# Performance work log

Measured on AMD Instinct MI355X. Metric: run time of the kernel, lower is better.

Reference implementation:

```python
import jax, jax.numpy as jnp
import numpy as np

THR = 1.0  # snntorch Leaky default threshold
BETA = 0.9


def setup_inputs() -> dict:
    key = jax.random.key(0)
    k_in, k_w1, k_b1, k_w2, k_b2 = jax.random.split(key, 5)
    T, B, D, H = 100, 256, 784, 256
    # binary spike train input (rate-coded)
    spike_input = (jax.random.uniform(k_in, (T, B, D)) < 0.5).astype(jnp.float32)
    # nn.Linear init: U(-1/sqrt(fan_in), 1/sqrt(fan_in))
    lim1 = 1.0 / np.sqrt(D)
    lim2 = 1.0 / np.sqrt(H)
    W1 = jax.random.uniform(k_w1, (H, D), minval=-lim1, maxval=lim1, dtype=jnp.float32)
    b1 = jax.random.uniform(k_b1, (H,), minval=-lim1, maxval=lim1, dtype=jnp.float32)
    W2 = jax.random.uniform(k_w2, (D, H), minval=-lim2, maxval=lim2, dtype=jnp.float32)
    b2 = jax.random.uniform(k_b2, (D,), minval=-lim2, maxval=lim2, dtype=jnp.float32)
    return {"spike_input": spike_input, "W1": W1, "b1": b1, "W2": W2, "b2": b2}


def _heaviside(x):
    return (x > 0).astype(x.dtype)


def reference(spike_input, W1, b1, W2, b2):
    T, B, D = spike_input.shape
    H = W1.shape[0]

    def step(carry, x_t):
        mem1, mem2 = carry
        # layer 1: Linear + Leaky LIF (reset-by-subtraction, as in snntorch)
        cur1 = x_t @ W1.T + b1                          # [B,H]
        reset1 = _heaviside(mem1 - THR)                 # spikes from previous mem
        mem1 = BETA * mem1 + cur1 - reset1 * THR
        spk1 = _heaviside(mem1 - THR)
        # layer 2
        cur2 = spk1 @ W2.T + b2                         # [B,D]
        reset2 = _heaviside(mem2 - THR)
        mem2 = BETA * mem2 + cur2 - reset2 * THR
        spk2 = _heaviside(mem2 - THR)
        return (mem1, mem2), spk2

    mem1_0 = jnp.zeros((B, H), dtype=spike_input.dtype)
    mem2_0 = jnp.zeros((B, D), dtype=spike_input.dtype)
    _, spk_out = jax.lax.scan(step, (mem1_0, mem2_0), spike_input)
    return spk_out  # [T,B,D]
```

## Files before the change

kernel.cpp:

```cpp
#include <hip/hip_runtime.h>

typedef __attribute__((ext_vector_type(8))) _Float16 f16x8;
typedef __attribute__((ext_vector_type(4))) float f32x4;

static constexpr int TT = 100, BB = 256, DD = 784, HH = 256;
static constexpr int MM = TT * BB;
static constexpr int K1PAD = 800;
static constexpr int N2PAD = 800;
static constexpr float MIDSC = 2048.0f, INVMID = 1.0f / 2048.0f;

__device__ __forceinline__ unsigned short f2h(float x) {
  _Float16 h = (_Float16)x;
  return *(unsigned short*)&h;
}
__device__ __forceinline__ float h2f(unsigned short u) {
  _Float16 h = *(_Float16*)&u;
  return (float)h;
}
__device__ __forceinline__ void glds16(const void* g, void* l) {
  __builtin_amdgcn_global_load_lds(
      (const __attribute__((address_space(1))) unsigned int*)g,
      (__attribute__((address_space(3))) unsigned int*)l, 16, 0, 0);
}

__global__ __launch_bounds__(256)
void split_w(const float* __restrict__ W, unsigned short* __restrict__ Ws,
             int N, int K, int Npad, int Kpad) {
  int idx = blockIdx.x * 256 + threadIdx.x;
  int total = Npad * Kpad;
  if (idx >= total) return;
  int row = idx / Kpad, col = idx - row * Kpad;
  float w = (row < N && col < K) ? W[row * K + col] : 0.0f;
  unsigned short h0 = f2h(w);
  float r = (w - h2f(h0)) * MIDSC;
  Ws[idx] = h0;
  Ws[total + idx] = f2h(r);
}

__global__ __launch_bounds__(256, 2)
void gemm1(const float* __restrict__ X, const unsigned short* __restrict__ Bs,
           const float* __restrict__ bias, float* __restrict__ C) {
  constexpr int Kpad = K1PAD, nkb = Kpad / 32;
  __shared__ unsigned short Asm[2][128 * 32];
  __shared__ unsigned short Bsm[3][2][128 * 32];
  const int tid = threadIdx.x;
  const int bm = blockIdx.x * 128, bn = blockIdx.y * 128;
  const int wid = tid >> 6, lane = tid & 63;
  const int wr = (wid >> 1) * 64, wc = (wid & 1) * 64;
  const int l15 = lane & 15, l4 = lane >> 4;

  f32x4 acc[2][4][4];
#pragma unroll
  for (int s = 0; s < 2; ++s)
#pragma unroll
    for (int m = 0; m < 4; ++m)
#pragma unroll
      for (int n = 0; n < 4; ++n) acc[s][m][n] = (f32x4){0.f, 0.f, 0.f, 0.f};

  const int rl = wid * 32 + (lane >> 2);
  const int ce = ((lane & 3) ^ ((lane >> 3) & 3)) * 8;
  const size_t pstr = (size_t)HH * Kpad;
  const unsigned short* bsrc0 = Bs + (size_t)(bn + rl) * Kpad + ce;
  const unsigned short* bsrc1 = Bs + (size_t)(bn + rl + 16) * Kpad + ce;

  const int rdsw = (l4 ^ ((l15 >> 1) & 3)) * 8;

  const int r0 = tid >> 2;
  const int c0log = (tid & 3) * 8;
  const int c0phys = ((tid & 3) ^ ((tid >> 3) & 3)) * 8;

  float4 aA[4], aB[4];

  auto loadA = [&](int kb, float4 (&d)[4]) {
    const int col = kb * 32 + c0log;
    const bool ok = col < DD;
    const int colc = ok ? col : 0;
    const float* p0 = &X[(size_t)(bm + r0) * DD + colc];
    const float* p1 = &X[(size_t)(bm + r0 + 64) * DD + colc];
    d[0] = *(const float4*)p0; d[1] = *(const float4*)(p0 + 4);
    d[2] = *(const float4*)p1; d[3] = *(const float4*)(p1 + 4);
    if (!ok) {
      const float4 z = make_float4(0.f, 0.f, 0.f, 0.f);
      d[0] = z; d[1] = z; d[2] = z; d[3] = z;
    }
  };
  auto packA = [&](int bi, const float4 (&s_)[4]) {
    const unsigned ONE = 0x3C00u;
    auto pk = [&](float a, float b) {
      return (a != 0.f ? ONE : 0u) | (b != 0.f ? (ONE << 16) : 0u);
    };
    uint4 v0, v1;
    v0.x = pk(s_[0].x, s_[0].y); v0.y = pk(s_[0].z, s_[0].w);
    v0.z = pk(s_[1].x, s_[1].y); v0.w = pk(s_[1].z, s_[1].w);
    v1.x = pk(s_[2].x, s_[2].y); v1.y = pk(s_[2].z, s_[2].w);
    v1.z = pk(s_[3].x, s_[3].y); v1.w = pk(s_[3].z, s_[3].w);
    *(uint4*)&Asm[bi][r0 * 32 + c0phys] = v0;
    *(uint4*)&Asm[bi][(r0 + 64) * 32 + c0phys] = v1;
  };
  auto stageB = [&](int t) {
    const int k0 = t * 32, bi = t % 3;
    glds16(bsrc0 + k0, &Bsm[bi][0][(wid * 32) * 32]);
    glds16(bsrc1 + k0, &Bsm[bi][0][(wid * 32 + 16) * 32]);
    glds16(bsrc0 + pstr + k0, &Bsm[bi][1][(wid * 32) * 32]);
    glds16(bsrc1 + pstr + k0, &Bsm[bi][1][(wid * 32 + 16) * 32]);
  };
  auto compute = [&](int kb) {
    const int cb = kb & 1, b3 = kb % 3;
    f16x8 afr[4];
#pragma unroll
    for (int m = 0; m < 4; ++m)
      afr[m] = *(const f16x8*)&Asm[cb][(wr + m * 16 + l15) * 32 + rdsw];
#pragma unroll
    for (int s = 0; s < 2; ++s) {
      f16x8 bfr[4];
#pragma unroll
      for (int n = 0; n < 4; ++n)
        bfr[n] = *(const f16x8*)&Bsm[b3][s][(wc + n * 16 + l15) * 32 + rdsw];
#pragma unroll
      for (int m = 0; m < 4; ++m)
#pragma unroll
        for (int n = 0; n < 4; ++n)
          acc[s][m][n] = __builtin_amdgcn_mfma_f32_16x16x32_f16(afr[m], bfr[n], acc[s][m][n], 0, 0, 0);
    }
  };
  auto stepK = [&](int kb, const float4 (&pk_)[4], float4 (&ld_)[4]) {
    if (kb + 1 < nkb) packA((kb + 1) & 1, pk_);
    if (kb + 2 < nkb) stageB(kb + 2);
    compute(kb);
    __builtin_amdgcn_sched_barrier(0);
    if (kb + 2 < nkb) asm volatile("s_waitcnt vmcnt(4)" ::: "memory");
    else              asm volatile("s_waitcnt vmcnt(0)" ::: "memory");
    if (kb + 2 < nkb) loadA(kb + 2, ld_);
    asm volatile("s_waitcnt lgkmcnt(0)" ::: "memory");
    __builtin_amdgcn_sched_barrier(0);
    __builtin_amdgcn_s_barrier();
    __builtin_amdgcn_sched_barrier(0);
  };

  loadA(0, aA);
  stageB(0); stageB(1);
  asm volatile("s_waitcnt vmcnt(8)" ::: "memory");
  packA(0, aA);
  loadA(1, aB);
  asm volatile("s_waitcnt vmcnt(8)" ::: "memory");
  asm volatile("s_waitcnt lgkmcnt(0)" ::: "memory");
  __builtin_amdgcn_s_barrier();
  __builtin_amdgcn_sched_barrier(0);

  for (int kb2 = 0; kb2 < nkb; kb2 += 2) {
    stepK(kb2, aB, aA);
    if (kb2 + 1 < nkb) stepK(kb2 + 1, aA, aB);
  }

#pragma unroll
  for (int m = 0; m < 4; ++m)
#pragma unroll
    for (int n = 0; n < 4; ++n) {
      const int col = bn + wc + n * 16 + l15;
      const float bv = bias[col];
#pragma unroll
      for (int r = 0; r < 4; ++r) {
        const int row = bm + wr + m * 16 + l4 * 4 + r;
        C[(size_t)row * HH + col] = fmaf(acc[1][m][n][r], INVMID, acc[0][m][n][r]) + bv;
      }
    }
}

__global__ __launch_bounds__(256)
void lif_scan_h4(const float4* __restrict__ cur, uint2* __restrict__ spk,
                 int NE4, int nt) {
  const int tid = blockIdx.x * 256 + threadIdx.x;
  float4 mem = make_float4(0.f, 0.f, 0.f, 0.f);
  auto step1 = [](float& m, float c) {
    const float reset = (m > 1.0f) ? 1.0f : 0.0f;
    m = __fsub_rn(__fadd_rn(__fmul_rn(0.9f, m), c), reset);
    return (m > 1.0f);
  };
#pragma unroll 4
  for (int t = 0; t < nt; ++t) {
    const float4 c = cur[(size_t)t * NE4 + tid];
    unsigned s0 = step1(mem.x, c.x) ? 0x3C00u : 0u;
    unsigned s1 = step1(mem.y, c.y) ? 0x3C00u : 0u;
    unsigned s2 = step1(mem.z, c.z) ? 0x3C00u : 0u;
    unsigned s3 = step1(mem.w, c.w) ? 0x3C00u : 0u;
    uint2 o;
    o.x = s0 | (s1 << 16);
    o.y = s2 | (s3 << 16);
    spk[(size_t)t * NE4 + tid] = o;
  }
}

__global__ __launch_bounds__(64)
void fused_l2(const unsigned short* __restrict__ spk1,
              const unsigned short* __restrict__ W2s,
              const float* __restrict__ b2, float* __restrict__ out) {
  __shared__ unsigned short Asm[4][16 * 256];
  const int lane = threadIdx.x;
  const int l15 = lane & 15, l4 = lane >> 4;
  const int bb = blockIdx.x / 49, dd = blockIdx.x - bb * 49;
  const int b0 = bb * 16, d0 = dd * 16;

  const unsigned short* asrc[8];
#pragma unroll
  for (int i = 0; i < 8; ++i) {
    const int r = 2 * i + (lane >> 5);
    const int e = ((lane & 31) * 8) ^ ((r & 7) << 3);
    asrc[i] = spk1 + (size_t)(b0 + r) * HH + e;
  }
  auto stageA = [&](int t) {
    const size_t toff = (size_t)t * (BB * HH);
    unsigned short* dst = &Asm[t & 3][0];
#pragma unroll
    for (int i = 0; i < 8; ++i)
      glds16(asrc[i] + toff, dst + 2 * i * 256);
  };

  stageA(0);
  stageA(1);

  f16x8 wfr[2][8];
  const unsigned short* wb = W2s + (size_t)(d0 + l15) * HH + l4 * 8;
#pragma unroll
  for (int s = 0; s < 2; ++s)
#pragma unroll
    for (int ks = 0; ks < 8; ++ks)
      wfr[s][ks] = *(const f16x8*)(wb + (size_t)s * (N2PAD * HH) + ks * 32);
  const float bv = b2[d0 + l15];

  asm volatile("s_waitcnt vmcnt(0)" ::: "memory");
  __builtin_amdgcn_sched_barrier(0);

  f32x4 mem = (f32x4){0.f, 0.f, 0.f, 0.f};
  float* obase = out + (size_t)(b0 + l4 * 4) * DD + d0 + l15;

  int roff[8];
#pragma unroll
  for (int ks = 0; ks < 8; ++ks)
    roff[ks] = l15 * 256 + ((ks * 32 + l4 * 8) ^ ((l15 & 7) << 3));

  for (int p = 0; p < TT; p += 2) {
    if (p + 2 < TT) { stageA(p + 2); stageA(p + 3); }
    if (p == 0)            asm volatile("s_waitcnt vmcnt(16)" ::: "memory");
    else if (p + 2 < TT)   asm volatile("s_waitcnt vmcnt(24)" ::: "memory");
    else                   asm volatile("s_waitcnt vmcnt(8)"  ::: "memory");
    __builtin_amdgcn_sched_barrier(0);

    const unsigned short* bufA = &Asm[p & 3][0];
    const unsigned short* bufB = &Asm[(p + 1) & 3][0];

    f16x8 rA[8];
#pragma unroll
    for (int ks = 0; ks < 8; ++ks)
      rA[ks] = *(const f16x8*)&bufA[roff[ks]];
    f32x4 p0a = (f32x4){0.f, 0.f, 0.f, 0.f}, p0b = p0a, p1a = p0a, p1b = p0a;
#pragma unroll
    for (int ks = 0; ks < 4; ++ks) {
      p0a = __builtin_amdgcn_mfma_f32_16x16x32_f16(rA[ks], wfr[0][ks], p0a, 0, 0, 0);
      p1a = __builtin_amdgcn_mfma_f32_16x16x32_f16(rA[ks], wfr[1][ks], p1a, 0, 0, 0);
    }
#pragma unroll
    for (int ks = 4; ks < 8; ++ks) {
      p0b = __builtin_amdgcn_mfma_f32_16x16x32_f16(rA[ks], wfr[0][ks], p0b, 0, 0, 0);
      p1b = __builtin_amdgcn_mfma_f32_16x16x32_f16(rA[ks], wfr[1][ks], p1b, 0, 0, 0);
    }

    f16x8 rB[8];
#pragma unroll
    for (int ks = 0; ks < 8; ++ks)
      rB[ks] = *(const f16x8*)&bufB[roff[ks]];

    {
      float* op = obase + (size_t)p * ((size_t)BB * DD);
#pragma unroll
      for (int r = 0; r < 4; ++r) {
        const float p0 = p0a[r] + p0b[r];
        const float p1 = p1a[r] + p1b[r];
        const float cur = fmaf(p1, INVMID, p0) + bv;
        const float reset = (mem[r] > 1.0f) ? 1.0f : 0.0f;
        mem[r] = __fsub_rn(__fadd_rn(__fmul_rn(0.9f, mem[r]), cur), reset);
        op[(size_t)r * DD] = (mem[r] > 1.0f) ? 1.0f : 0.0f;
      }
    }

    f32x4 q0a = (f32x4){0.f, 0.f, 0.f, 0.f}, q0b = q0a, q1a = q0a, q1b = q0a;
#pragma unroll
    for (int ks = 0; ks < 4; ++ks) {
      q0a = __builtin_amdgcn_mfma_f32_16x16x32_f16(rB[ks], wfr[0][ks], q0a, 0, 0, 0);
      q1a = __builtin_amdgcn_mfma_f32_16x16x32_f16(rB[ks], wfr[1][ks], q1a, 0, 0, 0);
    }
#pragma unroll
    for (int ks = 4; ks < 8; ++ks) {
      q0b = __builtin_amdgcn_mfma_f32_16x16x32_f16(rB[ks], wfr[0][ks], q0b, 0, 0, 0);
      q1b = __builtin_amdgcn_mfma_f32_16x16x32_f16(rB[ks], wfr[1][ks], q1b, 0, 0, 0);
    }
    {
      float* op = obase + (size_t)(p + 1) * ((size_t)BB * DD);
#pragma unroll
      for (int r = 0; r < 4; ++r) {
        const float p0 = q0a[r] + q0b[r];
        const float p1 = q1a[r] + q1b[r];
        const float cur = fmaf(p1, INVMID, p0) + bv;
        const float reset = (mem[r] > 1.0f) ? 1.0f : 0.0f;
        mem[r] = __fsub_rn(__fadd_rn(__fmul_rn(0.9f, mem[r]), cur), reset);
        op[(size_t)r * DD] = (mem[r] > 1.0f) ? 1.0f : 0.0f;
      }
    }
  }
}

extern "C" void kernel_launch(void* const* d_in, const int* in_sizes, int n_in,
                              void* d_out, int out_size, void* d_ws, size_t ws_size,
                              hipStream_t stream) {
  const float* x  = (const float*)d_in[0];
  const float* W1 = (const float*)d_in[1];
  const float* b1 = (const float*)d_in[2];
  const float* W2 = (const float*)d_in[3];
  const float* b2 = (const float*)d_in[4];
  float* out = (float*)d_out;

  const size_t w1s_elems = (size_t)2 * HH * K1PAD;
  const size_t w2s_elems = (size_t)2 * N2PAD * HH;
  unsigned short* W1s = (unsigned short*)d_ws;
  unsigned short* W2s = W1s + w1s_elems;
  float* cur1 = (float*)(W2s + w2s_elems);
  unsigned short* spk1 = (unsigned short*)(cur1 + (size_t)MM * HH);

  dim3 blk(256);

  split_w<<<dim3((HH * K1PAD + 255) / 256), blk, 0, stream>>>(W1, W1s, HH, DD, HH, K1PAD);
  split_w<<<dim3((N2PAD * HH + 255) / 256), blk, 0, stream>>>(W2, W2s, DD, HH, N2PAD, HH);

  gemm1<<<dim3(MM / 128, HH / 128), blk, 0, stream>>>(x, W1s, b1, cur1);

  lif_scan_h4<<<dim3((BB * HH / 4) / 256), blk, 0, stream>>>(
      (const float4*)cur1, (uint2*)spk1, BB * HH / 4, TT);

  fused_l2<<<dim3(16 * 49), dim3(64), 0, stream>>>(spk1, W2s, b2, out);
}
```

Baseline: 106.4 us.

## Deepen gemm1 software pipeline to three-stage prefetch for A and B

Adds a fourth B shared-memory buffer and a third A register buffer so that global loads for A and B are issued three K-blocks ahead instead of two, and reorders issue so the loads go out before packing and compute. Waitcnt thresholds are retuned to match the deeper queue. The goal is to hide more global-memory latency behind the MFMA work, at the cost of more LDS and register pressure, which may reduce occupancy under the 2-blocks-per-CU launch bound.

```diff
diff --git a/kernel.cpp b/kernel.cpp
--- a/kernel.cpp
+++ b/kernel.cpp
@@ -42,7 +42,7 @@
            const float* __restrict__ bias, float* __restrict__ C) {
   constexpr int Kpad = K1PAD, nkb = Kpad / 32;
   __shared__ unsigned short Asm[2][128 * 32];
-  __shared__ unsigned short Bsm[3][2][128 * 32];
+  __shared__ unsigned short Bsm[4][2][128 * 32];
   const int tid = threadIdx.x;
   const int bm = blockIdx.x * 128, bn = blockIdx.y * 128;
   const int wid = tid >> 6, lane = tid & 63;
@@ -69,7 +69,7 @@
   const int c0log = (tid & 3) * 8;
   const int c0phys = ((tid & 3) ^ ((tid >> 3) & 3)) * 8;
 
-  float4 aA[4], aB[4];
+  float4 a0[4], a1[4], a2[4];
 
   auto loadA = [&](int kb, float4 (&d)[4]) {
     const int col = kb * 32 + c0log;
@@ -98,14 +98,14 @@
     *(uint4*)&Asm[bi][(r0 + 64) * 32 + c0phys] = v1;
   };
   auto stageB = [&](int t) {
-    const int k0 = t * 32, bi = t % 3;
+    const int k0 = t * 32, bi = t & 3;
     glds16(bsrc0 + k0, &Bsm[bi][0][(wid * 32) * 32]);
     glds16(bsrc1 + k0, &Bsm[bi][0][(wid * 32 + 16) * 32]);
     glds16(bsrc0 + pstr + k0, &Bsm[bi][1][(wid * 32) * 32]);
     glds16(bsrc1 + pstr + k0, &Bsm[bi][1][(wid * 32 + 16) * 32]);
   };
   auto compute = [&](int kb) {
-    const int cb = kb & 1, b3 = kb % 3;
+    const int cb = kb & 1, b4 = kb & 3;
     f16x8 afr[4];
 #pragma unroll
     for (int m = 0; m < 4; ++m)
@@ -115,7 +115,7 @@
       f16x8 bfr[4];
 #pragma unroll
       for (int n = 0; n < 4; ++n)
-        bfr[n] = *(const f16x8*)&Bsm[b3][s][(wc + n * 16 + l15) * 32 + rdsw];
+        bfr[n] = *(const f16x8*)&Bsm[b4][s][(wc + n * 16 + l15) * 32 + rdsw];
 #pragma unroll
       for (int m = 0; m < 4; ++m)
 #pragma unroll
@@ -123,33 +123,35 @@
           acc[s][m][n] = __builtin_amdgcn_mfma_f32_16x16x32_f16(afr[m], bfr[n], acc[s][m][n], 0, 0, 0);
     }
   };
-  auto stepK = [&](int kb, const float4 (&pk_)[4], float4 (&ld_)[4]) {
+  auto stepK = [&](int kb, float4 (&ld)[4], const float4 (&pk_)[4]) {
+    if (kb + 3 < nkb) loadA(kb + 3, ld);
+    if (kb + 3 < nkb) stageB(kb + 3);
     if (kb + 1 < nkb) packA((kb + 1) & 1, pk_);
-    if (kb + 2 < nkb) stageB(kb + 2);
     compute(kb);
     __builtin_amdgcn_sched_barrier(0);
-    if (kb + 2 < nkb) asm volatile("s_waitcnt vmcnt(4)" ::: "memory");
-    else              asm volatile("s_waitcnt vmcnt(0)" ::: "memory");
-    if (kb + 2 < nkb) loadA(kb + 2, ld_);
+    if (kb == 0)           asm volatile("s_waitcnt vmcnt(12)" ::: "memory");
+    else if (kb + 3 < nkb) asm volatile("s_waitcnt vmcnt(16)" ::: "memory");
+    else if (kb + 2 < nkb) asm volatile("s_waitcnt vmcnt(8)"  ::: "memory");
+    else                   asm volatile("s_waitcnt vmcnt(0)"  ::: "memory");
     asm volatile("s_waitcnt lgkmcnt(0)" ::: "memory");
     __builtin_amdgcn_sched_barrier(0);
     __builtin_amdgcn_s_barrier();
     __builtin_amdgcn_sched_barrier(0);
   };
 
-  loadA(0, aA);
-  stageB(0); stageB(1);
-  asm volatile("s_waitcnt vmcnt(8)" ::: "memory");
-  packA(0, aA);
-  loadA(1, aB);
+  loadA(0, a0); loadA(1, a1); loadA(2, a2);
+  stageB(0); stageB(1); stageB(2);
+  asm volatile("s_waitcnt vmcnt(20)" ::: "memory");
+  packA(0, a0);
   asm volatile("s_waitcnt vmcnt(8)" ::: "memory");
   asm volatile("s_waitcnt lgkmcnt(0)" ::: "memory");
   __builtin_amdgcn_s_barrier();
   __builtin_amdgcn_sched_barrier(0);
 
-  for (int kb2 = 0; kb2 < nkb; kb2 += 2) {
-    stepK(kb2, aB, aA);
-    if (kb2 + 1 < nkb) stepK(kb2 + 1, aA, aB);
+  for (int kb = 0; kb < nkb; kb += 3) {
+    stepK(kb, a0, a1);
+    if (kb + 1 < nkb) stepK(kb + 1, a1, a2);
+    if (kb + 2 < nkb) stepK(kb + 2, a2, a0);
   }
 
 #pragma unroll
```

After: 111.6 us. 1.05x slower.

## Use 512-thread blocks in gemm1 with smaller per-wave tiles

Applied to the files above, without the earlier changes.

The gemm1 block grows from 4 to 8 waves, and each wave now computes a 32x64 output tile instead of 64x64. The A and B staging work is spread over all 512 threads, so each thread issues half as many loads, and the vmcnt waits are lowered to match. The goal is fewer accumulator registers per thread and more waves per CU to hide memory latency. The cost is more LDS fragment reads per MFMA and more barrier participants per block.

```diff
diff --git a/kernel.cpp b/kernel.cpp
--- a/kernel.cpp
+++ b/kernel.cpp
@@ -37,7 +37,7 @@
   Ws[total + idx] = f2h(r);
 }
 
-__global__ __launch_bounds__(256, 2)
+__global__ __launch_bounds__(512, 4)
 void gemm1(const float* __restrict__ X, const unsigned short* __restrict__ Bs,
            const float* __restrict__ bias, float* __restrict__ C) {
   constexpr int Kpad = K1PAD, nkb = Kpad / 32;
@@ -46,22 +46,24 @@
   const int tid = threadIdx.x;
   const int bm = blockIdx.x * 128, bn = blockIdx.y * 128;
   const int wid = tid >> 6, lane = tid & 63;
-  const int wr = (wid >> 1) * 64, wc = (wid & 1) * 64;
+  const int wr = (wid & 3) * 32;
+  const int wc = (wid >> 2) * 64;
   const int l15 = lane & 15, l4 = lane >> 4;
 
-  f32x4 acc[2][4][4];
+  f32x4 acc[2][2][4];
 #pragma unroll
   for (int s = 0; s < 2; ++s)
 #pragma unroll
-    for (int m = 0; m < 4; ++m)
+    for (int m = 0; m < 2; ++m)
 #pragma unroll
       for (int n = 0; n < 4; ++n) acc[s][m][n] = (f32x4){0.f, 0.f, 0.f, 0.f};
 
-  const int rl = wid * 32 + (lane >> 2);
+  const int bp = wid >> 2, br = (wid & 3) * 32;
+  const int rl = br + (lane >> 2);
   const int ce = ((lane & 3) ^ ((lane >> 3) & 3)) * 8;
   const size_t pstr = (size_t)HH * Kpad;
-  const unsigned short* bsrc0 = Bs + (size_t)(bn + rl) * Kpad + ce;
-  const unsigned short* bsrc1 = Bs + (size_t)(bn + rl + 16) * Kpad + ce;
+  const unsigned short* bsrc0 = Bs + (size_t)bp * pstr + (size_t)(bn + rl) * Kpad + ce;
+  const unsigned short* bsrc1 = bsrc0 + (size_t)16 * Kpad;
 
   const int rdsw = (l4 ^ ((l15 >> 1) & 3)) * 8;
 
@@ -69,46 +71,39 @@
   const int c0log = (tid & 3) * 8;
   const int c0phys = ((tid & 3) ^ ((tid >> 3) & 3)) * 8;
 
-  float4 aA[4], aB[4];
-
-  auto loadA = [&](int kb, float4 (&d)[4]) {
+  float4 aA[2], aB[2];
+
+  auto loadA = [&](int kb, float4 (&d)[2]) {
     const int col = kb * 32 + c0log;
-    const bool ok = col < DD;
-    const int colc = ok ? col : 0;
-    const float* p0 = &X[(size_t)(bm + r0) * DD + colc];
-    const float* p1 = &X[(size_t)(bm + r0 + 64) * DD + colc];
-    d[0] = *(const float4*)p0; d[1] = *(const float4*)(p0 + 4);
-    d[2] = *(const float4*)p1; d[3] = *(const float4*)(p1 + 4);
-    if (!ok) {
-      const float4 z = make_float4(0.f, 0.f, 0.f, 0.f);
-      d[0] = z; d[1] = z; d[2] = z; d[3] = z;
-    }
-  };
-  auto packA = [&](int bi, const float4 (&s_)[4]) {
+    if (col < DD) {
+      const float* p = &X[(size_t)(bm + r0) * DD + col];
+      d[0] = *(const float4*)p;
+      d[1] = *(const float4*)(p + 4);
+    } else {
+      d[0] = make_float4(0.f, 0.f, 0.f, 0.f);
+      d[1] = d[0];
+    }
+  };
+  auto packA = [&](int bi, const float4 (&s_)[2]) {
     const unsigned ONE = 0x3C00u;
     auto pk = [&](float a, float b) {
       return (a != 0.f ? ONE : 0u) | (b != 0.f ? (ONE << 16) : 0u);
     };
-    uint4 v0, v1;
-    v0.x = pk(s_[0].x, s_[0].y); v0.y = pk(s_[0].z, s_[0].w);
-    v0.z = pk(s_[1].x, s_[1].y); v0.w = pk(s_[1].z, s_[1].w);
-    v1.x = pk(s_[2].x, s_[2].y); v1.y = pk(s_[2].z, s_[2].w);
-    v1.z = pk(s_[3].x, s_[3].y); v1.w = pk(s_[3].z, s_[3].w);
-    *(uint4*)&Asm[bi][r0 * 32 + c0phys] = v0;
-    *(uint4*)&Asm[bi][(r0 + 64) * 32 + c0phys] = v1;
+    uint4 v;
+    v.x = pk(s_[0].x, s_[0].y); v.y = pk(s_[0].z, s_[0].w);
+    v.z = pk(s_[1].x, s_[1].y); v.w = pk(s_[1].z, s_[1].w);
+    *(uint4*)&Asm[bi][r0 * 32 + c0phys] = v;
   };
   auto stageB = [&](int t) {
     const int k0 = t * 32, bi = t % 3;
-    glds16(bsrc0 + k0, &Bsm[bi][0][(wid * 32) * 32]);
-    glds16(bsrc1 + k0, &Bsm[bi][0][(wid * 32 + 16) * 32]);
-    glds16(bsrc0 + pstr + k0, &Bsm[bi][1][(wid * 32) * 32]);
-    glds16(bsrc1 + pstr + k0, &Bsm[bi][1][(wid * 32 + 16) * 32]);
+    glds16(bsrc0 + k0, &Bsm[bi][bp][br * 32]);
+    glds16(bsrc1 + k0, &Bsm[bi][bp][(br + 16) * 32]);
   };
   auto compute = [&](int kb) {
     const int cb = kb & 1, b3 = kb % 3;
-    f16x8 afr[4];
-#pragma unroll
-    for (int m = 0; m < 4; ++m)
+    f16x8 afr[2];
+#pragma unroll
+    for (int m = 0; m < 2; ++m)
       afr[m] = *(const f16x8*)&Asm[cb][(wr + m * 16 + l15) * 32 + rdsw];
 #pragma unroll
     for (int s = 0; s < 2; ++s) {
@@ -117,18 +112,18 @@
       for (int n = 0; n < 4; ++n)
         bfr[n] = *(const f16x8*)&Bsm[b3][s][(wc + n * 16 + l15) * 32 + rdsw];
 #pragma unroll
-      for (int m = 0; m < 4; ++m)
+      for (int m = 0; m < 2; ++m)
 #pragma unroll
         for (int n = 0; n < 4; ++n)
           acc[s][m][n] = __builtin_amdgcn_mfma_f32_16x16x32_f16(afr[m], bfr[n], acc[s][m][n], 0, 0, 0);
     }
   };
-  auto stepK = [&](int kb, const float4 (&pk_)[4], float4 (&ld_)[4]) {
+  auto stepK = [&](int kb, const float4 (&pk_)[2], float4 (&ld_)[2]) {
     if (kb + 1 < nkb) packA((kb + 1) & 1, pk_);
     if (kb + 2 < nkb) stageB(kb + 2);
     compute(kb);
     __builtin_amdgcn_sched_barrier(0);
-    if (kb + 2 < nkb) asm volatile("s_waitcnt vmcnt(4)" ::: "memory");
+    if (kb + 2 < nkb) asm volatile("s_waitcnt vmcnt(2)" ::: "memory");
     else              asm volatile("s_waitcnt vmcnt(0)" ::: "memory");
     if (kb + 2 < nkb) loadA(kb + 2, ld_);
     asm volatile("s_waitcnt lgkmcnt(0)" ::: "memory");
@@ -139,10 +134,10 @@
 
   loadA(0, aA);
   stageB(0); stageB(1);
-  asm volatile("s_waitcnt vmcnt(8)" ::: "memory");
+  asm volatile("s_waitcnt vmcnt(4)" ::: "memory");
   packA(0, aA);
   loadA(1, aB);
-  asm volatile("s_waitcnt vmcnt(8)" ::: "memory");
+  asm volatile("s_waitcnt vmcnt(4)" ::: "memory");
   asm volatile("s_waitcnt lgkmcnt(0)" ::: "memory");
   __builtin_amdgcn_s_barrier();
   __builtin_amdgcn_sched_barrier(0);
@@ -153,7 +148,7 @@
   }
 
 #pragma unroll
-  for (int m = 0; m < 4; ++m)
+  for (int m = 0; m < 2; ++m)
 #pragma unroll
     for (int n = 0; n < 4; ++n) {
       const int col = bn + wc + n * 16 + l15;
@@ -330,7 +325,7 @@
   split_w<<<dim3((HH * K1PAD + 255) / 256), blk, 0, stream>>>(W1, W1s, HH, DD, HH, K1PAD);
   split_w<<<dim3((N2PAD * HH + 255) / 256), blk, 0, stream>>>(W2, W2s, DD, HH, N2PAD, HH);
 
-  gemm1<<<dim3(MM / 128, HH / 128), blk, 0, stream>>>(x, W1s, b1, cur1);
+  gemm1<<<dim3(MM / 128, HH / 128), dim3(512), 0, stream>>>(x, W1s, b1, cur1);
 
   lif_scan_h4<<<dim3((BB * HH / 4) / 256), blk, 0, stream>>>(
       (const float4*)cur1, (uint2*)spk1, BB * HH / 4, TT);
```

Result: slower. 152.9 us (+43.7%).

## Double the gemm1 K-tile to 64 with a reworked double-buffered pipeline

Applied to the files above, without the earlier changes.

The layer-1 GEMM now processes 64-wide K tiles instead of 32, and K is padded from 800 to 832 so it divides evenly. The triple-buffered B stage becomes double-buffered with an 8-way XOR swizzle. A moves to a padded row stride (72) in place of the swizzle, and the next A global load is issued before the MFMA compute. The aim is to halve the number of barriers and pipeline steps and give each step more MFMAs for hiding latency. In exchange, LDS use and register pressure rise, occupancy drops to one block per CU, and about 4% more padded zero work is done.

```diff
diff --git a/kernel.cpp b/kernel.cpp
--- a/kernel.cpp
+++ b/kernel.cpp
@@ -5,7 +5,7 @@
 
 static constexpr int TT = 100, BB = 256, DD = 784, HH = 256;
 static constexpr int MM = TT * BB;
-static constexpr int K1PAD = 800;
+static constexpr int K1PAD = 832;
 static constexpr int N2PAD = 800;
 static constexpr float MIDSC = 2048.0f, INVMID = 1.0f / 2048.0f;
 
@@ -37,12 +37,13 @@
   Ws[total + idx] = f2h(r);
 }
 
-__global__ __launch_bounds__(256, 2)
+__global__ __launch_bounds__(256, 1)
 void gemm1(const float* __restrict__ X, const unsigned short* __restrict__ Bs,
            const float* __restrict__ bias, float* __restrict__ C) {
-  constexpr int Kpad = K1PAD, nkb = Kpad / 32;
-  __shared__ unsigned short Asm[2][128 * 32];
-  __shared__ unsigned short Bsm[3][2][128 * 32];
+  constexpr int Kpad = K1PAD, nkb = Kpad / 64;
+  constexpr int AST = 72;
+  __shared__ unsigned short Asm[2][128 * AST];
+  __shared__ unsigned short Bsm[2][2][128 * 64];
   const int tid = threadIdx.x;
   const int bm = blockIdx.x * 128, bn = blockIdx.y * 128;
   const int wid = tid >> 6, lane = tid & 63;
@@ -57,80 +58,84 @@
 #pragma unroll
       for (int n = 0; n < 4; ++n) acc[s][m][n] = (f32x4){0.f, 0.f, 0.f, 0.f};
 
-  const int rl = wid * 32 + (lane >> 2);
-  const int ce = ((lane & 3) ^ ((lane >> 3) & 3)) * 8;
+  const int gp = wid >> 1, gr = (wid & 1) * 64;
   const size_t pstr = (size_t)HH * Kpad;
-  const unsigned short* bsrc0 = Bs + (size_t)(bn + rl) * Kpad + ce;
-  const unsigned short* bsrc1 = Bs + (size_t)(bn + rl + 16) * Kpad + ce;
-
-  const int rdsw = (l4 ^ ((l15 >> 1) & 3)) * 8;
-
-  const int r0 = tid >> 2;
-  const int c0log = (tid & 3) * 8;
-  const int c0phys = ((tid & 3) ^ ((tid >> 3) & 3)) * 8;
-
-  float4 aA[4], aB[4];
-
-  auto loadA = [&](int kb, float4 (&d)[4]) {
-    const int col = kb * 32 + c0log;
-    const bool ok = col < DD;
-    const int colc = ok ? col : 0;
-    const float* p0 = &X[(size_t)(bm + r0) * DD + colc];
-    const float* p1 = &X[(size_t)(bm + r0 + 64) * DD + colc];
-    d[0] = *(const float4*)p0; d[1] = *(const float4*)(p0 + 4);
-    d[2] = *(const float4*)p1; d[3] = *(const float4*)(p1 + 4);
-    if (!ok) {
-      const float4 z = make_float4(0.f, 0.f, 0.f, 0.f);
-      d[0] = z; d[1] = z; d[2] = z; d[3] = z;
-    }
-  };
-  auto packA = [&](int bi, const float4 (&s_)[4]) {
+  const unsigned short* bsrc = Bs + (size_t)gp * pstr
+      + (size_t)(bn + gr + (lane >> 3)) * Kpad
+      + ((lane & 7) ^ ((lane >> 3) & 7)) * 8;
+
+  const int r0 = tid & 127;
+  const int cb = (tid >> 7) * 32;
+
+  float4 aA[8], aB[8];
+
+  auto loadA = [&](int kb, float4 (&d)[8]) {
+    const float* xr = &X[(size_t)(bm + r0) * DD];
+#pragma unroll
+    for (int c = 0; c < 4; ++c) {
+      const int col = kb * 64 + cb + c * 8;
+      if (col < DD) {
+        d[2 * c]     = *(const float4*)(xr + col);
+        d[2 * c + 1] = *(const float4*)(xr + col + 4);
+      } else {
+        d[2 * c] = make_float4(0.f, 0.f, 0.f, 0.f);
+        d[2 * c + 1] = d[2 * c];
+      }
+    }
+  };
+  auto packA = [&](int bi, const float4 (&s_)[8]) {
     const unsigned ONE = 0x3C00u;
     auto pk = [&](float a, float b) {
       return (a != 0.f ? ONE : 0u) | (b != 0.f ? (ONE << 16) : 0u);
     };
-    uint4 v0, v1;
-    v0.x = pk(s_[0].x, s_[0].y); v0.y = pk(s_[0].z, s_[0].w);
-    v0.z = pk(s_[1].x, s_[1].y); v0.w = pk(s_[1].z, s_[1].w);
-    v1.x = pk(s_[2].x, s_[2].y); v1.y = pk(s_[2].z, s_[2].w);
-    v1.z = pk(s_[3].x, s_[3].y); v1.w = pk(s_[3].z, s_[3].w);
-    *(uint4*)&Asm[bi][r0 * 32 + c0phys] = v0;
-    *(uint4*)&Asm[bi][(r0 + 64) * 32 + c0phys] = v1;
+#pragma unroll
+    for (int c = 0; c < 4; ++c) {
+      uint4 v;
+      v.x = pk(s_[2 * c].x, s_[2 * c].y);
+      v.y = pk(s_[2 * c].z, s_[2 * c].w);
+      v.z = pk(s_[2 * c + 1].x, s_[2 * c + 1].y);
+      v.w = pk(s_[2 * c + 1].z, s_[2 * c + 1].w);
+      *(uint4*)&Asm[bi][r0 * AST + cb + c * 8] = v;
+    }
   };
   auto stageB = [&](int t) {
-    const int k0 = t * 32, bi = t % 3;
-    glds16(bsrc0 + k0, &Bsm[bi][0][(wid * 32) * 32]);
-    glds16(bsrc1 + k0, &Bsm[bi][0][(wid * 32 + 16) * 32]);
-    glds16(bsrc0 + pstr + k0, &Bsm[bi][1][(wid * 32) * 32]);
-    glds16(bsrc1 + pstr + k0, &Bsm[bi][1][(wid * 32 + 16) * 32]);
+    const int bi = t & 1;
+    const unsigned short* src = bsrc + t * 64;
+#pragma unroll
+    for (int i = 0; i < 8; ++i)
+      glds16(src + (size_t)i * 8 * Kpad, &Bsm[bi][gp][(gr + i * 8) * 64]);
   };
   auto compute = [&](int kb) {
-    const int cb = kb & 1, b3 = kb % 3;
-    f16x8 afr[4];
-#pragma unroll
-    for (int m = 0; m < 4; ++m)
-      afr[m] = *(const f16x8*)&Asm[cb][(wr + m * 16 + l15) * 32 + rdsw];
-#pragma unroll
-    for (int s = 0; s < 2; ++s) {
-      f16x8 bfr[4];
-#pragma unroll
-      for (int n = 0; n < 4; ++n)
-        bfr[n] = *(const f16x8*)&Bsm[b3][s][(wc + n * 16 + l15) * 32 + rdsw];
+    const int bi = kb & 1;
+#pragma unroll
+    for (int ks = 0; ks < 2; ++ks) {
+      f16x8 afr[4];
 #pragma unroll
       for (int m = 0; m < 4; ++m)
+        afr[m] = *(const f16x8*)&Asm[bi][(wr + m * 16 + l15) * AST + ks * 32 + l4 * 8];
+#pragma unroll
+      for (int s = 0; s < 2; ++s) {
+        f16x8 bfr[4];
 #pragma unroll
         for (int n = 0; n < 4; ++n)
-          acc[s][m][n] = __builtin_amdgcn_mfma_f32_16x16x32_f16(afr[m], bfr[n], acc[s][m][n], 0, 0, 0);
-    }
-  };
-  auto stepK = [&](int kb, const float4 (&pk_)[4], float4 (&ld_)[4]) {
+          bfr[n] = *(const f16x8*)&Bsm[bi][s][(wc + n * 16 + l15) * 64
+                    + ((ks * 4 + l4) ^ (l15 & 7)) * 8];
+#pragma unroll
+        for (int m = 0; m < 4; ++m)
+#pragma unroll
+          for (int n = 0; n < 4; ++n)
+            acc[s][m][n] = __builtin_amdgcn_mfma_f32_16x16x32_f16(afr[m], bfr[n], acc[s][m][n], 0, 0, 0);
+      }
+    }
+  };
+  auto stepK = [&](int kb, const float4 (&pk_)[8], float4 (&ld_)[8]) {
     if (kb + 1 < nkb) packA((kb + 1) & 1, pk_);
-    if (kb + 2 < nkb) stageB(kb + 2);
+    if (kb + 1 < nkb) stageB(kb + 1);
+    if (kb + 2 < nkb) loadA(kb + 2, ld_);
     compute(kb);
     __builtin_amdgcn_sched_barrier(0);
-    if (kb + 2 < nkb) asm volatile("s_waitcnt vmcnt(4)" ::: "memory");
-    else              asm volatile("s_waitcnt vmcnt(0)" ::: "memory");
-    if (kb + 2 < nkb) loadA(kb + 2, ld_);
+    if (kb + 2 < nkb)      asm volatile("s_waitcnt vmcnt(8)" ::: "memory");
+    else                   asm volatile("s_waitcnt vmcnt(0)" ::: "memory");
     asm volatile("s_waitcnt lgkmcnt(0)" ::: "memory");
     __builtin_amdgcn_sched_barrier(0);
     __builtin_amdgcn_s_barrier();
@@ -138,8 +143,8 @@
   };
 
   loadA(0, aA);
-  stageB(0); stageB(1);
-  asm volatile("s_waitcnt vmcnt(8)" ::: "memory");
+  stageB(0);
+  asm volatile("s_waitcnt vmcnt(32)" ::: "memory");
   packA(0, aA);
   loadA(1, aB);
   asm volatile("s_waitcnt vmcnt(8)" ::: "memory");
```

Result: slower. 206.7 us (+94.2%).
